# Performance work log

Measured on AMD Instinct MI355X. Metric: run time of the kernel, lower is better.

The kernel has to match this reference:

```python
import jax, jax.numpy as jnp
import numpy as np

B, LQ, LK, E, H, TOPK = 8, 512, 2048, 512, 8, 20
HD = E // H  # head dim = 64


def setup_inputs() -> dict:
    key = jax.random.key(0)
    ks = jax.random.split(key, 8)
    s = 1.0 / np.sqrt(E)
    return {
        "q": jax.random.normal(ks[0], (B, LQ, E), jnp.float32),
        "k": jax.random.normal(ks[1], (B, LK, E), jnp.float32),
        "v": jax.random.normal(ks[2], (B, LK, E), jnp.float32),
        "Wq": jax.random.normal(ks[3], (E, E), jnp.float32) * s,
        "Wk": jax.random.normal(ks[4], (E, E), jnp.float32) * s,
        "Wv": jax.random.normal(ks[5], (E, E), jnp.float32) * s,
        "Wo": jax.random.normal(ks[6], (E, E), jnp.float32) * s,
        "bo": jnp.zeros((E,), jnp.float32),
    }


def reference(q, k, v, Wq, Wk, Wv, Wo, bo):
    # torch Linear: y = x @ W^T
    def heads(x, W, L):
        return (x @ W.T).reshape(B, L, H, HD).transpose(0, 2, 1, 3)  # [B,H,L,HD]

    query = heads(q, Wq, LQ)
    key_ = heads(k, Wk, LK)
    value = heads(v, Wv, LK)

    scores = jnp.einsum("bhqd,bhkd->bhqk", query, key_) / np.sqrt(HD)
    scores = jax.nn.softmax(scores, axis=-1)  # [B,H,LQ,LK]

    topk_vals, topk_idx = jax.lax.top_k(scores, TOPK)  # [B,H,LQ,K]

    # scatter top-k probs back into a sparse weight matrix (rest zero)
    bi = jnp.arange(B)[:, None, None, None]
    hi = jnp.arange(H)[None, :, None, None]
    qi = jnp.arange(LQ)[None, None, :, None]
    attn = jnp.zeros_like(scores).at[bi, hi, qi, topk_idx].set(topk_vals)

    out = jnp.einsum("bhqk,bhkd->bhqd", attn, value)
    out = out.transpose(0, 2, 1, 3).reshape(B, LQ, E)
    return out @ Wo.T + bo + q
```

## Files before the change

kernel.cpp:

```cpp
#include <hip/hip_runtime.h>
#include <hip/hip_bf16.h>

#define NB 8
#define LQ 512
#define LK 2048
#define EE 512
#define NH 8
#define HD 64
#define NTOPK 20

typedef float f4v __attribute__((ext_vector_type(4)));
typedef short s8v __attribute__((ext_vector_type(8)));
typedef __bf16 bfrag __attribute__((ext_vector_type(8)));

__device__ inline short f2bf(float f) {
    union { float f; unsigned u; } x; x.f = f;
    unsigned r = (x.u + 0x7FFFu + ((x.u >> 16) & 1u)) >> 16;
    return (short)r;
}
__device__ inline float bf2f(short s) {
    union { unsigned u; float f; } x;
    x.u = ((unsigned)(unsigned short)s) << 16;
    return x.f;
}
__device__ inline float exp2_fast(float x) {
    float r;
    asm("v_exp_f32 %0, %1" : "=v"(r) : "v"(x));
    return r;
}

__device__ inline unsigned wave_max_u32(unsigned x) {
    unsigned t;
    t = (unsigned)__builtin_amdgcn_update_dpp(0, (int)x, 0x111, 0xf, 0xf, true); x = x > t ? x : t;
    t = (unsigned)__builtin_amdgcn_update_dpp(0, (int)x, 0x112, 0xf, 0xf, true); x = x > t ? x : t;
    t = (unsigned)__builtin_amdgcn_update_dpp(0, (int)x, 0x114, 0xf, 0xf, true); x = x > t ? x : t;
    t = (unsigned)__builtin_amdgcn_update_dpp(0, (int)x, 0x118, 0xf, 0xf, true); x = x > t ? x : t;
    t = (unsigned)__builtin_amdgcn_update_dpp(0, (int)x, 0x142, 0xf, 0xf, true); x = x > t ? x : t;
    t = (unsigned)__builtin_amdgcn_update_dpp(0, (int)x, 0x143, 0xf, 0xf, true); x = x > t ? x : t;
    return (unsigned)__builtin_amdgcn_readlane((int)x, 63);
}
__device__ inline float wave_sum_f32(float x) {
    union fi { float f; int i; } a, t;
    a.f = x;
    t.i = __builtin_amdgcn_update_dpp(0, a.i, 0x111, 0xf, 0xf, true); a.f += t.f;
    t.i = __builtin_amdgcn_update_dpp(0, a.i, 0x112, 0xf, 0xf, true); a.f += t.f;
    t.i = __builtin_amdgcn_update_dpp(0, a.i, 0x114, 0xf, 0xf, true); a.f += t.f;
    t.i = __builtin_amdgcn_update_dpp(0, a.i, 0x118, 0xf, 0xf, true); a.f += t.f;
    t.i = __builtin_amdgcn_update_dpp(0, a.i, 0x142, 0xf, 0xf, true); a.f += t.f;
    t.i = __builtin_amdgcn_update_dpp(0, a.i, 0x143, 0xf, 0xf, true); a.f += t.f;
    a.i = __builtin_amdgcn_readlane(a.i, 63);
    return a.f;
}

__global__ __launch_bounds__(256) void cvt_all(
    const float* __restrict__ q, const float* __restrict__ k, const float* __restrict__ v,
    const float* __restrict__ wq, const float* __restrict__ wk, const float* __restrict__ wv,
    const float* __restrict__ wo,
    short* __restrict__ qb, short* __restrict__ kb, short* __restrict__ vb,
    short* __restrict__ wqb, short* __restrict__ wkb, short* __restrict__ wvb,
    short* __restrict__ wob)
{
    const float* src; short* dst; int n;
    switch (blockIdx.y) {
        case 0: src = q;  dst = qb;  n = NB * LQ * EE; break;
        case 1: src = k;  dst = kb;  n = NB * LK * EE; break;
        case 2: src = v;  dst = vb;  n = NB * LK * EE; break;
        case 3: src = wq; dst = wqb; n = EE * EE; break;
        case 4: src = wk; dst = wkb; n = EE * EE; break;
        case 5: src = wv; dst = wvb; n = EE * EE; break;
        default: src = wo; dst = wob; n = EE * EE; break;
    }
    const int nv = n >> 3;
    for (int i = blockIdx.x * 256 + threadIdx.x; i < nv; i += gridDim.x * 256) {
        f4v a = *(const f4v*)&src[(size_t)i * 8];
        f4v b = *(const f4v*)&src[(size_t)i * 8 + 4];
        s8v o;
        o[0] = f2bf(a[0]); o[1] = f2bf(a[1]); o[2] = f2bf(a[2]); o[3] = f2bf(a[3]);
        o[4] = f2bf(b[0]); o[5] = f2bf(b[1]); o[6] = f2bf(b[2]); o[7] = f2bf(b[3]);
        *(s8v*)&dst[(size_t)i * 8] = o;
    }
}

template<int MODE>
__global__ __launch_bounds__(256) void gemm_bf16(
    const short* __restrict__ A, const short* __restrict__ W,
    void* __restrict__ C, const float* __restrict__ bias,
    const float* __restrict__ resid)
{
    __shared__ short As[128][72];
    __shared__ short Bs[128][72];
    const int tid  = threadIdx.x;
    const int lane = tid & 63;
    const int wr   = (tid >> 7) & 1;
    const int wc   = (tid >> 6) & 1;
    const size_t bm = (size_t)blockIdx.y * 128;
    const int    bn = blockIdx.x * 128;

    f4v acc[4][4] = {};
    const int lr  = lane & 15;
    const int kg  = (lane >> 4) * 8;
    const int srow = tid >> 3;
    const int sc8  = (tid & 7) * 8;

    for (int ks = 0; ks < EE; ks += 64) {
        #pragma unroll
        for (int i = 0; i < 4; i++) {
            const int row = i * 32 + srow;
            *(s8v*)&As[row][sc8] = *(const s8v*)&A[(bm + row) * EE + ks + sc8];
            *(s8v*)&Bs[row][sc8] = *(const s8v*)&W[(size_t)(bn + row) * EE + ks + sc8];
        }
        __syncthreads();
        #pragma unroll
        for (int kk = 0; kk < 64; kk += 32) {
            bfrag af[4], bf[4];
            #pragma unroll
            for (int mi = 0; mi < 4; mi++)
                af[mi] = *(const bfrag*)&As[wr * 64 + mi * 16 + lr][kk + kg];
            #pragma unroll
            for (int ni = 0; ni < 4; ni++)
                bf[ni] = *(const bfrag*)&Bs[wc * 64 + ni * 16 + lr][kk + kg];
            #pragma unroll
            for (int mi = 0; mi < 4; mi++)
                #pragma unroll
                for (int ni = 0; ni < 4; ni++)
                    acc[mi][ni] = __builtin_amdgcn_mfma_f32_16x16x32_bf16(
                        af[mi], bf[ni], acc[mi][ni], 0, 0, 0);
        }
        __syncthreads();
    }

    const int rj = (lane >> 4) * 4;
    #pragma unroll
    for (int mi = 0; mi < 4; mi++) {
        #pragma unroll
        for (int ni = 0; ni < 4; ni++) {
            const int    col  = bn + wc * 64 + ni * 16 + lr;
            const size_t row0 = bm + wr * 64 + mi * 16 + rj;
            #pragma unroll
            for (int j = 0; j < 4; j++) {
                const float  v   = acc[mi][ni][j];
                const size_t idx = (row0 + j) * EE + col;
                if (MODE == 0) ((short*)C)[idx] = f2bf(v);
                else           ((float*)C)[idx] = v + bias[col] + resid[idx];
            }
        }
    }
}

__global__ __launch_bounds__(256) void score_gemm(
    const short* __restrict__ Qp, const short* __restrict__ Kp,
    short* __restrict__ Sg)
{
    __shared__ short As[128][72];
    __shared__ short Bs[128][72];
    const int tid  = threadIdx.x;
    const int lane = tid & 63;
    const int wr   = (tid >> 7) & 1;
    const int wc   = (tid >> 6) & 1;
    const int z  = blockIdx.z;
    const int h  = z & 7;
    const int b  = z >> 3;
    const int bm = blockIdx.y * 128;
    const int bn = blockIdx.x * 128;

    const short* Ab = Qp + (size_t)b * LQ * EE + h * HD;
    const short* Bb = Kp + (size_t)b * LK * EE + h * HD;

    #pragma unroll
    for (int i = 0; i < 4; i++) {
        const int row = i * 32 + (tid >> 3);
        const int c8  = (tid & 7) * 8;
        *(s8v*)&As[row][c8] = *(const s8v*)&Ab[(size_t)(bm + row) * EE + c8];
        *(s8v*)&Bs[row][c8] = *(const s8v*)&Bb[(size_t)(bn + row) * EE + c8];
    }
    __syncthreads();

    f4v acc[4][4] = {};
    const int lr = lane & 15;
    const int kg = (lane >> 4) * 8;
    #pragma unroll
    for (int kk = 0; kk < HD; kk += 32) {
        bfrag af[4], bf[4];
        #pragma unroll
        for (int mi = 0; mi < 4; mi++)
            af[mi] = *(const bfrag*)&As[wr * 64 + mi * 16 + lr][kk + kg];
        #pragma unroll
        for (int ni = 0; ni < 4; ni++)
            bf[ni] = *(const bfrag*)&Bs[wc * 64 + ni * 16 + lr][kk + kg];
        #pragma unroll
        for (int mi = 0; mi < 4; mi++)
            #pragma unroll
            for (int ni = 0; ni < 4; ni++)
                acc[mi][ni] = __builtin_amdgcn_mfma_f32_16x16x32_bf16(
                    af[mi], bf[ni], acc[mi][ni], 0, 0, 0);
    }

    short* Sh = Sg + (size_t)z * LQ * LK;
    const int rj = (lane >> 4) * 4;
    #pragma unroll
    for (int mi = 0; mi < 4; mi++) {
        #pragma unroll
        for (int ni = 0; ni < 4; ni++) {
            const int col = bn + wc * 64 + ni * 16 + lr;
            const int r0  = bm + wr * 64 + mi * 16 + rj;
            #pragma unroll
            for (int j = 0; j < 4; j++)
                Sh[(size_t)(r0 + j) * LK + col] = f2bf(acc[mi][ni][j] * 0.18033688f);
        }
    }
}

__global__ __launch_bounds__(256) void topk_pv(
    const unsigned short* __restrict__ Sg, const short* __restrict__ Vp,
    short* __restrict__ attn)
{
    __shared__ unsigned wkey[4][NTOPK];
    __shared__ float    wp[4][NTOPK];
    __shared__ unsigned widx[4][NTOPK];
    const int lane = threadIdx.x & 63;
    const int wid  = threadIdx.x >> 6;
    const int r  = blockIdx.x * 4 + wid;
    const int h  = (r >> 9) & 7;
    const int qi = r & 511;
    const int b  = r >> 12;
    const unsigned short* Srow = Sg + (size_t)r * LK;

    s8v raw[4];
    #pragma unroll
    for (int t = 0; t < 4; t++)
        raw[t] = *(const s8v*)&Srow[t * 512 + lane * 8];

    const unsigned invl = 2047u - (unsigned)(lane * 8);
    unsigned v1 = 0, v2 = 0, v3 = 0;
    #pragma unroll
    for (int t = 0; t < 4; t++) {
        #pragma unroll
        for (int e = 0; e < 8; e++) {
            const unsigned u   = (unsigned short)raw[t][e];
            const unsigned sgn = (unsigned)((int)(u << 16) >> 31);
            const unsigned kc  = ((u ^ (0x8000u | (sgn & 0x7FFFu))) << 11)
                               | (invl - (unsigned)(t * 512 + e));
            const unsigned m1 = v1 < kc ? v1 : kc;
            v1 = v1 > kc ? v1 : kc;
            const unsigned m2 = v2 < m1 ? v2 : m1;
            v2 = v2 > m1 ? v2 : m1;
            v3 = v3 > m2 ? v3 : m2;
        }
    }

    unsigned K = wave_max_u32(v1);
    const unsigned mtop  = K >> 11;
    const unsigned mbits = (mtop & 0x8000u) ? (mtop ^ 0x8000u) : (~mtop & 0xFFFFu);
    union { unsigned u; float f; } mu; mu.u = mbits << 16;
    const float M = mu.f;

    float sum = 0.f;
    #pragma unroll
    for (int t = 0; t < 4; t++)
        #pragma unroll
        for (int e = 0; e < 8; e++)
            sum += exp2_fast(bf2f(raw[t][e]) - M);
    sum = wave_sum_f32(sum);
    const float inv = 1.f / sum;

    unsigned rm = 0;
    #pragma unroll 1
    for (int kk = 0; kk < NTOPK; kk++) {
        if (lane == 0) wkey[wid][kk] = K;
        if (v1 == K) {
            const unsigned idx  = 2047u - (K & 2047u);
            const unsigned slot = ((idx >> 9) << 3) | (idx & 7u);
            rm |= (1u << slot);
            v1 = v2; v2 = v3; v3 = 0;
        }
        if (__any(v1 == 0u)) {
            if (v1 == 0u) {
                unsigned a1 = 0, a2 = 0, a3 = 0;
                #pragma unroll
                for (int t = 0; t < 4; t++) {
                    #pragma unroll
                    for (int e = 0; e < 8; e++) {
                        const int c = t * 8 + e;
                        const unsigned u   = (unsigned short)raw[t][e];
                        const unsigned sgn = (unsigned)((int)(u << 16) >> 31);
                        unsigned kc = ((u ^ (0x8000u | (sgn & 0x7FFFu))) << 11)
                                    | (invl - (unsigned)(t * 512 + e));
                        kc = ((rm >> c) & 1u) ? 0u : kc;
                        const unsigned m1 = a1 < kc ? a1 : kc;
                        a1 = a1 > kc ? a1 : kc;
                        const unsigned m2 = a2 < m1 ? a2 : m1;
                        a2 = a2 > m1 ? a2 : m1;
                        a3 = a3 > m2 ? a3 : m2;
                    }
                }
                v1 = a1; v2 = a2; v3 = a3;
            }
        }
        K = wave_max_u32(v1);
    }

    __syncthreads();
    if (lane < NTOPK) {
        const unsigned Kk  = wkey[wid][lane];
        const unsigned idx = 2047u - (Kk & 2047u);
        const unsigned mo  = Kk >> 11;
        const unsigned sb  = (mo & 0x8000u) ? (mo ^ 0x8000u) : (~mo & 0xFFFFu);
        union { unsigned u; float f; } su; su.u = sb << 16;
        wp[wid][lane]   = exp2_fast(su.f - M) * inv;
        widx[wid][lane] = idx;
    }
    __syncthreads();

    float oacc = 0.f;
    const short* Vb = Vp + (size_t)b * LK * EE + h * HD + lane;
    #pragma unroll
    for (int kk = 0; kk < NTOPK; kk++)
        oacc += wp[wid][kk] * bf2f(Vb[(size_t)widx[wid][kk] * EE]);

    attn[((size_t)b * LQ + qi) * EE + h * HD + lane] = f2bf(oacc);
}

extern "C" void kernel_launch(void* const* d_in, const int* in_sizes, int n_in,
                              void* d_out, int out_size, void* d_ws, size_t ws_size,
                              hipStream_t stream)
{
    const float* q  = (const float*)d_in[0];
    const float* k  = (const float*)d_in[1];
    const float* v  = (const float*)d_in[2];
    const float* Wq = (const float*)d_in[3];
    const float* Wk = (const float*)d_in[4];
    const float* Wv = (const float*)d_in[5];
    const float* Wo = (const float*)d_in[6];
    const float* bo = (const float*)d_in[7];

    if (ws_size < ((size_t)208 << 20)) return;

    char*  ws  = (char*)d_ws;
    short* qb  = (short*)(ws);
    short* kb  = (short*)(ws + ((size_t)4   << 20));
    short* vb  = (short*)(ws + ((size_t)20  << 20));
    short* wqb = (short*)(ws + ((size_t)36  << 20));
    short* wkb = (short*)(ws + ((size_t)36  << 20) + (512 << 10));
    short* wvb = (short*)(ws + ((size_t)37  << 20));
    short* wob = (short*)(ws + ((size_t)37  << 20) + (512 << 10));
    short* Qp  = (short*)(ws + ((size_t)38  << 20));
    short* Kp  = (short*)(ws + ((size_t)42  << 20));
    short* Vp  = (short*)(ws + ((size_t)58  << 20));
    short* att = (short*)(ws + ((size_t)74  << 20));
    short* Sg  = (short*)(ws + ((size_t)80  << 20));

    dim3 blk(256);
    cvt_all<<<dim3(512, 7), blk, 0, stream>>>(q, k, v, Wq, Wk, Wv, Wo,
                                              qb, kb, vb, wqb, wkb, wvb, wob);

    gemm_bf16<0><<<dim3(4, 32),  blk, 0, stream>>>(qb, wqb, Qp, nullptr, nullptr);
    gemm_bf16<0><<<dim3(4, 128), blk, 0, stream>>>(kb, wkb, Kp, nullptr, nullptr);
    gemm_bf16<0><<<dim3(4, 128), blk, 0, stream>>>(vb, wvb, Vp, nullptr, nullptr);

    score_gemm<<<dim3(LK / 128, LQ / 128, NB * NH), blk, 0, stream>>>(Qp, Kp, Sg);
    topk_pv<<<dim3(NB * NH * LQ / 4), blk, 0, stream>>>((const unsigned short*)Sg, Vp, att);

    gemm_bf16<2><<<dim3(4, 32), blk, 0, stream>>>(att, wob, (float*)d_out, bo, q);
}
```

Before: 271.8 us.

## Use direct global-to-LDS loads with XOR swizzle and cheaper wave reductions in top-k

The GEMM and score kernels now load tiles with global_load_lds straight into an unpadded, XOR-swizzled LDS layout instead of going through registers. This removes register staging and the padding, and the swizzle is meant to avoid bank conflicts. The top-k softmax kernel now computes the exp-sum without subtracting the max, which relies on the score range not overflowing. It also replaces the DPP-plus-readlane reductions with butterfly all-reduces, keeps the selected keys in registers instead of LDS, and reads the weights and indices as vectors.

```diff
diff --git a/kernel.cpp b/kernel.cpp
--- a/kernel.cpp
+++ b/kernel.cpp
@@ -10,6 +10,7 @@
 #define NTOPK 20
 
 typedef float f4v __attribute__((ext_vector_type(4)));
+typedef unsigned u4v __attribute__((ext_vector_type(4)));
 typedef short s8v __attribute__((ext_vector_type(8)));
 typedef __bf16 bfrag __attribute__((ext_vector_type(8)));
 
@@ -29,26 +30,31 @@
     return r;
 }
 
-__device__ inline unsigned wave_max_u32(unsigned x) {
+__device__ inline void gld_lds16(const void* g, void* l) {
+    __builtin_amdgcn_global_load_lds(
+        (const __attribute__((address_space(1))) unsigned*)g,
+        (__attribute__((address_space(3))) unsigned*)l, 16, 0, 0);
+}
+
+__device__ inline unsigned wave_allmax_u32(unsigned x, int bpaddr) {
     unsigned t;
-    t = (unsigned)__builtin_amdgcn_update_dpp(0, (int)x, 0x111, 0xf, 0xf, true); x = x > t ? x : t;
-    t = (unsigned)__builtin_amdgcn_update_dpp(0, (int)x, 0x112, 0xf, 0xf, true); x = x > t ? x : t;
-    t = (unsigned)__builtin_amdgcn_update_dpp(0, (int)x, 0x114, 0xf, 0xf, true); x = x > t ? x : t;
-    t = (unsigned)__builtin_amdgcn_update_dpp(0, (int)x, 0x118, 0xf, 0xf, true); x = x > t ? x : t;
-    t = (unsigned)__builtin_amdgcn_update_dpp(0, (int)x, 0x142, 0xf, 0xf, true); x = x > t ? x : t;
-    t = (unsigned)__builtin_amdgcn_update_dpp(0, (int)x, 0x143, 0xf, 0xf, true); x = x > t ? x : t;
-    return (unsigned)__builtin_amdgcn_readlane((int)x, 63);
-}
-__device__ inline float wave_sum_f32(float x) {
+    t = (unsigned)__builtin_amdgcn_update_dpp(0, (int)x, 0xB1,  0xf, 0xf, true); x = x > t ? x : t;
+    t = (unsigned)__builtin_amdgcn_update_dpp(0, (int)x, 0x4E,  0xf, 0xf, true); x = x > t ? x : t;
+    t = (unsigned)__builtin_amdgcn_update_dpp(0, (int)x, 0x141, 0xf, 0xf, true); x = x > t ? x : t;
+    t = (unsigned)__builtin_amdgcn_update_dpp(0, (int)x, 0x140, 0xf, 0xf, true); x = x > t ? x : t;
+    t = (unsigned)__builtin_amdgcn_ds_swizzle((int)x, 0x401F);                   x = x > t ? x : t;
+    t = (unsigned)__builtin_amdgcn_ds_bpermute(bpaddr, (int)x);                  x = x > t ? x : t;
+    return x;
+}
+__device__ inline float wave_allsum_f32(float x, int bpaddr) {
     union fi { float f; int i; } a, t;
     a.f = x;
-    t.i = __builtin_amdgcn_update_dpp(0, a.i, 0x111, 0xf, 0xf, true); a.f += t.f;
-    t.i = __builtin_amdgcn_update_dpp(0, a.i, 0x112, 0xf, 0xf, true); a.f += t.f;
-    t.i = __builtin_amdgcn_update_dpp(0, a.i, 0x114, 0xf, 0xf, true); a.f += t.f;
-    t.i = __builtin_amdgcn_update_dpp(0, a.i, 0x118, 0xf, 0xf, true); a.f += t.f;
-    t.i = __builtin_amdgcn_update_dpp(0, a.i, 0x142, 0xf, 0xf, true); a.f += t.f;
-    t.i = __builtin_amdgcn_update_dpp(0, a.i, 0x143, 0xf, 0xf, true); a.f += t.f;
-    a.i = __builtin_amdgcn_readlane(a.i, 63);
+    t.i = __builtin_amdgcn_update_dpp(0, a.i, 0xB1,  0xf, 0xf, true); a.f += t.f;
+    t.i = __builtin_amdgcn_update_dpp(0, a.i, 0x4E,  0xf, 0xf, true); a.f += t.f;
+    t.i = __builtin_amdgcn_update_dpp(0, a.i, 0x141, 0xf, 0xf, true); a.f += t.f;
+    t.i = __builtin_amdgcn_update_dpp(0, a.i, 0x140, 0xf, 0xf, true); a.f += t.f;
+    t.i = __builtin_amdgcn_ds_swizzle(a.i, 0x401F);                   a.f += t.f;
+    t.i = __builtin_amdgcn_ds_bpermute(bpaddr, a.i);                  a.f += t.f;
     return a.f;
 }
 
@@ -81,44 +87,55 @@
     }
 }
 
+#define LDSW(arr, row, bytecol) \
+    (*(const bfrag*)((const char*)(arr) + (row) * 128 + ((bytecol) ^ (((row) & 7) << 4))))
+
 template<int MODE>
 __global__ __launch_bounds__(256) void gemm_bf16(
     const short* __restrict__ A, const short* __restrict__ W,
     void* __restrict__ C, const float* __restrict__ bias,
     const float* __restrict__ resid)
 {
-    __shared__ short As[128][72];
-    __shared__ short Bs[128][72];
+    __shared__ short As[128 * 64];
+    __shared__ short Bs[128 * 64];
     const int tid  = threadIdx.x;
     const int lane = tid & 63;
+    const int wid  = tid >> 6;
     const int wr   = (tid >> 7) & 1;
     const int wc   = (tid >> 6) & 1;
     const size_t bm = (size_t)blockIdx.y * 128;
     const int    bn = blockIdx.x * 128;
 
     f4v acc[4][4] = {};
-    const int lr  = lane & 15;
-    const int kg  = (lane >> 4) * 8;
-    const int srow = tid >> 3;
-    const int sc8  = (tid & 7) * 8;
+    const int lr = lane & 15;
+    const int kg = (lane >> 4) * 8;
+    const int srow = wid * 8 + (lane >> 3);
+    const int scol = (lane & 7) * 16;
 
     for (int ks = 0; ks < EE; ks += 64) {
         #pragma unroll
         for (int i = 0; i < 4; i++) {
-            const int row = i * 32 + srow;
-            *(s8v*)&As[row][sc8] = *(const s8v*)&A[(bm + row) * EE + ks + sc8];
-            *(s8v*)&Bs[row][sc8] = *(const s8v*)&W[(size_t)(bn + row) * EE + ks + sc8];
+            const int r  = i * 32 + srow;
+            const int gc = scol ^ ((r & 7) << 4);
+            gld_lds16((const char*)&A[(bm + r) * EE + ks] + gc,
+                      (char*)As + (i * 32 + wid * 8) * 128);
+            gld_lds16((const char*)&W[((size_t)bn + r) * EE + ks] + gc,
+                      (char*)Bs + (i * 32 + wid * 8) * 128);
         }
         __syncthreads();
         #pragma unroll
         for (int kk = 0; kk < 64; kk += 32) {
             bfrag af[4], bf[4];
             #pragma unroll
-            for (int mi = 0; mi < 4; mi++)
-                af[mi] = *(const bfrag*)&As[wr * 64 + mi * 16 + lr][kk + kg];
-            #pragma unroll
-            for (int ni = 0; ni < 4; ni++)
-                bf[ni] = *(const bfrag*)&Bs[wc * 64 + ni * 16 + lr][kk + kg];
+            for (int mi = 0; mi < 4; mi++) {
+                const int ar = wr * 64 + mi * 16 + lr;
+                af[mi] = LDSW(As, ar, (kk + kg) * 2);
+            }
+            #pragma unroll
+            for (int ni = 0; ni < 4; ni++) {
+                const int br = wc * 64 + ni * 16 + lr;
+                bf[ni] = LDSW(Bs, br, (kk + kg) * 2);
+            }
             #pragma unroll
             for (int mi = 0; mi < 4; mi++)
                 #pragma unroll
@@ -151,10 +168,11 @@
     const short* __restrict__ Qp, const short* __restrict__ Kp,
     short* __restrict__ Sg)
 {
-    __shared__ short As[128][72];
-    __shared__ short Bs[128][72];
+    __shared__ short As[128 * 64];
+    __shared__ short Bs[128 * 64];
     const int tid  = threadIdx.x;
     const int lane = tid & 63;
+    const int wid  = tid >> 6;
     const int wr   = (tid >> 7) & 1;
     const int wc   = (tid >> 6) & 1;
     const int z  = blockIdx.z;
@@ -166,12 +184,16 @@
     const short* Ab = Qp + (size_t)b * LQ * EE + h * HD;
     const short* Bb = Kp + (size_t)b * LK * EE + h * HD;
 
+    const int srow = wid * 8 + (lane >> 3);
+    const int scol = (lane & 7) * 16;
     #pragma unroll
     for (int i = 0; i < 4; i++) {
-        const int row = i * 32 + (tid >> 3);
-        const int c8  = (tid & 7) * 8;
-        *(s8v*)&As[row][c8] = *(const s8v*)&Ab[(size_t)(bm + row) * EE + c8];
-        *(s8v*)&Bs[row][c8] = *(const s8v*)&Bb[(size_t)(bn + row) * EE + c8];
+        const int r  = i * 32 + srow;
+        const int gc = scol ^ ((r & 7) << 4);
+        gld_lds16((const char*)&Ab[(size_t)(bm + r) * EE] + gc,
+                  (char*)As + (i * 32 + wid * 8) * 128);
+        gld_lds16((const char*)&Bb[(size_t)(bn + r) * EE] + gc,
+                  (char*)Bs + (i * 32 + wid * 8) * 128);
     }
     __syncthreads();
 
@@ -182,11 +204,15 @@
     for (int kk = 0; kk < HD; kk += 32) {
         bfrag af[4], bf[4];
         #pragma unroll
-        for (int mi = 0; mi < 4; mi++)
-            af[mi] = *(const bfrag*)&As[wr * 64 + mi * 16 + lr][kk + kg];
-        #pragma unroll
-        for (int ni = 0; ni < 4; ni++)
-            bf[ni] = *(const bfrag*)&Bs[wc * 64 + ni * 16 + lr][kk + kg];
+        for (int mi = 0; mi < 4; mi++) {
+            const int ar = wr * 64 + mi * 16 + lr;
+            af[mi] = LDSW(As, ar, (kk + kg) * 2);
+        }
+        #pragma unroll
+        for (int ni = 0; ni < 4; ni++) {
+            const int br = wc * 64 + ni * 16 + lr;
+            bf[ni] = LDSW(Bs, br, (kk + kg) * 2);
+        }
         #pragma unroll
         for (int mi = 0; mi < 4; mi++)
             #pragma unroll
@@ -214,9 +240,8 @@
     const unsigned short* __restrict__ Sg, const short* __restrict__ Vp,
     short* __restrict__ attn)
 {
-    __shared__ unsigned wkey[4][NTOPK];
-    __shared__ float    wp[4][NTOPK];
-    __shared__ unsigned widx[4][NTOPK];
+    __shared__ float    wp[4][24];
+    __shared__ unsigned widx[4][24];
     const int lane = threadIdx.x & 63;
     const int wid  = threadIdx.x >> 6;
     const int r  = blockIdx.x * 4 + wid;
@@ -224,11 +249,23 @@
     const int qi = r & 511;
     const int b  = r >> 12;
     const unsigned short* Srow = Sg + (size_t)r * LK;
+    const int bpaddr = (lane ^ 32) << 2;
 
     s8v raw[4];
     #pragma unroll
     for (int t = 0; t < 4; t++)
         raw[t] = *(const s8v*)&Srow[t * 512 + lane * 8];
+
+    float p0 = 0.f, p1 = 0.f, p2 = 0.f, p3 = 0.f;
+    #pragma unroll
+    for (int e = 0; e < 8; e++) {
+        p0 += exp2_fast(bf2f(raw[0][e]));
+        p1 += exp2_fast(bf2f(raw[1][e]));
+        p2 += exp2_fast(bf2f(raw[2][e]));
+        p3 += exp2_fast(bf2f(raw[3][e]));
+    }
+    float sum = wave_allsum_f32((p0 + p1) + (p2 + p3), bpaddr);
+    const float inv = __builtin_amdgcn_rcpf(sum);
 
     const unsigned invl = 2047u - (unsigned)(lane * 8);
     unsigned v1 = 0, v2 = 0, v3 = 0;
@@ -248,25 +285,11 @@
         }
     }
 
-    unsigned K = wave_max_u32(v1);
-    const unsigned mtop  = K >> 11;
-    const unsigned mbits = (mtop & 0x8000u) ? (mtop ^ 0x8000u) : (~mtop & 0xFFFFu);
-    union { unsigned u; float f; } mu; mu.u = mbits << 16;
-    const float M = mu.f;
-
-    float sum = 0.f;
-    #pragma unroll
-    for (int t = 0; t < 4; t++)
-        #pragma unroll
-        for (int e = 0; e < 8; e++)
-            sum += exp2_fast(bf2f(raw[t][e]) - M);
-    sum = wave_sum_f32(sum);
-    const float inv = 1.f / sum;
-
-    unsigned rm = 0;
+    unsigned K = wave_allmax_u32(v1, bpaddr);
+    unsigned rm = 0, mykey = 0;
     #pragma unroll 1
     for (int kk = 0; kk < NTOPK; kk++) {
-        if (lane == 0) wkey[wid][kk] = K;
+        mykey = (lane == kk) ? K : mykey;
         if (v1 == K) {
             const unsigned idx  = 2047u - (K & 2047u);
             const unsigned slot = ((idx >> 9) << 3) | (idx & 7u);
@@ -296,26 +319,30 @@
                 v1 = a1; v2 = a2; v3 = a3;
             }
         }
-        K = wave_max_u32(v1);
-    }
-
-    __syncthreads();
+        K = wave_allmax_u32(v1, bpaddr);
+    }
+
     if (lane < NTOPK) {
-        const unsigned Kk  = wkey[wid][lane];
-        const unsigned idx = 2047u - (Kk & 2047u);
-        const unsigned mo  = Kk >> 11;
+        const unsigned idx = 2047u - (mykey & 2047u);
+        const unsigned mo  = mykey >> 11;
         const unsigned sb  = (mo & 0x8000u) ? (mo ^ 0x8000u) : (~mo & 0xFFFFu);
         union { unsigned u; float f; } su; su.u = sb << 16;
-        wp[wid][lane]   = exp2_fast(su.f - M) * inv;
+        wp[wid][lane]   = exp2_fast(su.f) * inv;
         widx[wid][lane] = idx;
     }
     __syncthreads();
 
+    f4v pw[5]; u4v iw[5];
+    #pragma unroll
+    for (int j = 0; j < 5; j++) {
+        pw[j] = *(const f4v*)&wp[wid][j * 4];
+        iw[j] = *(const u4v*)&widx[wid][j * 4];
+    }
     float oacc = 0.f;
     const short* Vb = Vp + (size_t)b * LK * EE + h * HD + lane;
     #pragma unroll
     for (int kk = 0; kk < NTOPK; kk++)
-        oacc += wp[wid][kk] * bf2f(Vb[(size_t)widx[wid][kk] * EE]);
+        oacc += pw[kk >> 2][kk & 3] * bf2f(Vb[(size_t)iw[kk >> 2][kk & 3] * EE]);
 
     attn[((size_t)b * LQ + qi) * EE + h * HD + lane] = f2bf(oacc);
 }
```

Result: no change. 274.6 us (+1.0%).
